# Performance work log

Measured on AMD Instinct MI355X. Metric: run time of the kernel, lower is better.

Reference implementation:

```python
import jax, jax.numpy as jnp
import numpy as np
import math

def setup_inputs() -> dict:
    key = jax.random.key(0)
    k1, k2, k3 = jax.random.split(key, 3)
    B, N, C = 32, 1024, 768
    x = jax.random.normal(k1, (B, N, C), dtype=jnp.float32)
    W = jax.random.normal(k2, (4, C), dtype=jnp.float32) * 0.02  # conv1x1 weight [out=4, in=C]
    b = jax.random.normal(k3, (4,), dtype=jnp.float32) * 0.02
    return {"x": x, "W": W, "b": b}

def reference(x, W, b):
    B, N, C = x.shape
    H = int(math.isqrt(N))
    L = H * H
    # [B,N,C] -> [B,C,H,H]
    xi = jnp.transpose(x, (0, 2, 1)).reshape(B, C, H, H)
    # alpha = Conv1x1(AvgPool(x)) -> [B,4]
    pooled = jnp.mean(xi, axis=(2, 3))                      # [B,C]
    alpha = pooled @ W.T + b                                # [B,4]
    a = alpha[:, :, None, None]                             # [B,4,1,1]
    # CrossScan directions
    x0 = xi.reshape(B, C, L)                                # row-major scan
    x1 = jnp.transpose(xi, (0, 1, 3, 2)).reshape(B, C, L)   # col-major scan
    x2 = x0[:, :, ::-1]                                     # reversed row-major
    x3 = x1[:, :, ::-1]                                     # reversed col-major
    # gated weighted sum over the 4 scans (fused elementwise)
    y = a[:, 0] * x0 + a[:, 1] * x1 + a[:, 2] * x2 + a[:, 3] * x3  # [B,C,L]
    return jnp.transpose(y, (0, 2, 1))                      # [B,L,C]
```

## Files before the change

kernel.cpp:

```cpp
#include <hip/hip_runtime.h>

#define BB 32
#define NN 1024
#define CC 768
#define HH 32
#define NCHUNK 32
#define NPER (NN / NCHUNK)
#define C4 (CC / 4)

__global__ void pool_partial(const float* __restrict__ x, float* __restrict__ part) {
    const int blk = blockIdx.x;
    const int b   = blk / NCHUNK;
    const int ch  = blk % NCHUNK;
    const int tid = threadIdx.x;
    const float* xb = x + ((size_t)b * NN + (size_t)ch * NPER) * CC;
    float* pb = part + (size_t)blk * CC;
#pragma unroll
    for (int cc = 0; cc < 3; ++cc) {
        const int c = cc * 256 + tid;
        float s = 0.f;
#pragma unroll 4
        for (int n = 0; n < NPER; ++n) s += xb[(size_t)n * CC + c];
        pb[c] = s;
    }
}

__global__ void alpha_kernel(const float* __restrict__ part,
                             const float* __restrict__ W,
                             const float* __restrict__ bias,
                             float* __restrict__ alpha) {
    const int b = blockIdx.x;
    const int tid = threadIdx.x;
    float ak[4] = {0.f, 0.f, 0.f, 0.f};
#pragma unroll
    for (int cc = 0; cc < 3; ++cc) {
        const int c = cc * 256 + tid;
        float s = 0.f;
#pragma unroll 8
        for (int ch = 0; ch < NCHUNK; ++ch)
            s += part[((size_t)b * NCHUNK + ch) * CC + c];
#pragma unroll
        for (int k = 0; k < 4; ++k) ak[k] += s * W[k * CC + c];
    }
    const int lane = tid & 63;
    const int wid  = tid >> 6;
    __shared__ float red[4][4];
#pragma unroll
    for (int k = 0; k < 4; ++k) {
        float v = ak[k];
#pragma unroll
        for (int off = 32; off >= 1; off >>= 1) v += __shfl_down(v, off);
        if (lane == 0) red[wid][k] = v;
    }
    __syncthreads();
    if (tid < 4) {
        const float s = red[0][tid] + red[1][tid] + red[2][tid] + red[3][tid];
        alpha[b * 4 + tid] = s * (1.0f / (float)NN) + bias[tid];
    }
}

__global__ void merge(const float* __restrict__ x,
                      const float* __restrict__ alpha,
                      float* __restrict__ out) {
    const unsigned total = (unsigned)BB * NN * C4;
    const float4* __restrict__ x4 = (const float4*)x;
    float4* __restrict__ o4 = (float4*)out;
    for (unsigned idx = blockIdx.x * blockDim.x + threadIdx.x; idx < total;
         idx += gridDim.x * blockDim.x) {
        const unsigned c4 = idx % C4;
        const unsigned l  = (idx / C4) % NN;
        const unsigned b  = idx / (C4 * NN);
        const unsigned lt  = ((l & (HH - 1)) << 5) | (l >> 5);
        const unsigned lr  = (NN - 1) - l;
        const unsigned ltr = (NN - 1) - lt;
        const float4* xb = x4 + (size_t)b * NN * C4;
        const float a0 = alpha[b * 4 + 0];
        const float a1 = alpha[b * 4 + 1];
        const float a2 = alpha[b * 4 + 2];
        const float a3 = alpha[b * 4 + 3];
        const float4 v0 = xb[(size_t)l   * C4 + c4];
        const float4 v1 = xb[(size_t)lt  * C4 + c4];
        const float4 v2 = xb[(size_t)lr  * C4 + c4];
        const float4 v3 = xb[(size_t)ltr * C4 + c4];
        float4 r;
        r.x = a0 * v0.x + a1 * v1.x + a2 * v2.x + a3 * v3.x;
        r.y = a0 * v0.y + a1 * v1.y + a2 * v2.y + a3 * v3.y;
        r.z = a0 * v0.z + a1 * v1.z + a2 * v2.z + a3 * v3.z;
        r.w = a0 * v0.w + a1 * v1.w + a2 * v2.w + a3 * v3.w;
        o4[idx] = r;
    }
}

extern "C" void kernel_launch(void* const* d_in, const int* in_sizes, int n_in,
                              void* d_out, int out_size, void* d_ws, size_t ws_size,
                              hipStream_t stream) {
    const float* x    = (const float*)d_in[0];
    const float* W    = (const float*)d_in[1];
    const float* bias = (const float*)d_in[2];
    float* out = (float*)d_out;

    float* part  = (float*)d_ws;
    float* alpha = part + (size_t)BB * NCHUNK * CC;

    pool_partial<<<BB * NCHUNK, 256, 0, stream>>>(x, part);
    alpha_kernel<<<BB, 256, 0, stream>>>(part, W, bias, alpha);
    merge<<<2048, 256, 0, stream>>>(x, alpha, out);
}
```

Baseline: 239.5 us.

## Process scan-symmetry orbits together so each input row is loaded once

The merge kernel now assigns one block per (batch, position) and handles only the canonical member of each orbit {l, transpose(l), reverse(l), reverse-transpose(l)}. It loads the four rows once and writes all four outputs using permuted alpha weights, with nontemporal stores. This removes the redundant fourfold gather of the input. Pooling and alpha kernels are switched to float4-vectorized loads with 192-thread blocks. Most merge blocks exit early, adding launch overhead in exchange for lower memory traffic.

```diff
diff --git a/kernel.cpp b/kernel.cpp
--- a/kernel.cpp
+++ b/kernel.cpp
@@ -8,43 +8,44 @@
 #define NPER (NN / NCHUNK)
 #define C4 (CC / 4)
 
-__global__ void pool_partial(const float* __restrict__ x, float* __restrict__ part) {
-    const int blk = blockIdx.x;
-    const int b   = blk / NCHUNK;
-    const int ch  = blk % NCHUNK;
-    const int tid = threadIdx.x;
-    const float* xb = x + ((size_t)b * NN + (size_t)ch * NPER) * CC;
-    float* pb = part + (size_t)blk * CC;
-#pragma unroll
-    for (int cc = 0; cc < 3; ++cc) {
-        const int c = cc * 256 + tid;
-        float s = 0.f;
-#pragma unroll 4
-        for (int n = 0; n < NPER; ++n) s += xb[(size_t)n * CC + c];
-        pb[c] = s;
-    }
+typedef float f32x4 __attribute__((ext_vector_type(4)));
+
+__device__ __forceinline__ f32x4 f4_fma4(float a0, f32x4 v0, float a1, f32x4 v1,
+                                         float a2, f32x4 v2, float a3, f32x4 v3) {
+    return a0 * v0 + a1 * v1 + a2 * v2 + a3 * v3;
 }
 
-__global__ void alpha_kernel(const float* __restrict__ part,
-                             const float* __restrict__ W,
+__global__ void pool_partial(const f32x4* __restrict__ x4, f32x4* __restrict__ part4) {
+    const int blk = blockIdx.x;
+    const int b   = blk >> 5;
+    const int ch  = blk & 31;
+    const int t   = threadIdx.x;
+    const f32x4* xb = x4 + ((size_t)(b * NN + ch * NPER)) * C4 + t;
+    f32x4 s = {0.f, 0.f, 0.f, 0.f};
+#pragma unroll 8
+    for (int n = 0; n < NPER; ++n) s += xb[(size_t)n * C4];
+    part4[(size_t)blk * C4 + t] = s;
+}
+
+__global__ void alpha_kernel(const f32x4* __restrict__ part4,
+                             const f32x4* __restrict__ W4,
                              const float* __restrict__ bias,
                              float* __restrict__ alpha) {
     const int b = blockIdx.x;
-    const int tid = threadIdx.x;
-    float ak[4] = {0.f, 0.f, 0.f, 0.f};
+    const int t = threadIdx.x;
+    f32x4 s = {0.f, 0.f, 0.f, 0.f};
+#pragma unroll 8
+    for (int ch = 0; ch < NCHUNK; ++ch)
+        s += part4[((size_t)(b * NCHUNK + ch)) * C4 + t];
+    float ak[4];
 #pragma unroll
-    for (int cc = 0; cc < 3; ++cc) {
-        const int c = cc * 256 + tid;
-        float s = 0.f;
-#pragma unroll 8
-        for (int ch = 0; ch < NCHUNK; ++ch)
-            s += part[((size_t)b * NCHUNK + ch) * CC + c];
-#pragma unroll
-        for (int k = 0; k < 4; ++k) ak[k] += s * W[k * CC + c];
+    for (int k = 0; k < 4; ++k) {
+        const f32x4 w = W4[k * C4 + t];
+        ak[k] = s.x * w.x + s.y * w.y + s.z * w.z + s.w * w.w;
     }
-    const int lane = tid & 63;
-    const int wid  = tid >> 6;
-    __shared__ float red[4][4];
+    const int lane = t & 63;
+    const int wid  = t >> 6;
+    __shared__ float red[3][4];
 #pragma unroll
     for (int k = 0; k < 4; ++k) {
         float v = ak[k];
@@ -53,42 +54,39 @@
         if (lane == 0) red[wid][k] = v;
     }
     __syncthreads();
-    if (tid < 4) {
-        const float s = red[0][tid] + red[1][tid] + red[2][tid] + red[3][tid];
-        alpha[b * 4 + tid] = s * (1.0f / (float)NN) + bias[tid];
+    if (t < 4) {
+        const float s3 = red[0][t] + red[1][t] + red[2][t];
+        alpha[b * 4 + t] = s3 * (1.0f / (float)NN) + bias[t];
     }
 }
 
-__global__ void merge(const float* __restrict__ x,
+__global__ void merge(const f32x4* __restrict__ x4,
                       const float* __restrict__ alpha,
-                      float* __restrict__ out) {
-    const unsigned total = (unsigned)BB * NN * C4;
-    const float4* __restrict__ x4 = (const float4*)x;
-    float4* __restrict__ o4 = (float4*)out;
-    for (unsigned idx = blockIdx.x * blockDim.x + threadIdx.x; idx < total;
-         idx += gridDim.x * blockDim.x) {
-        const unsigned c4 = idx % C4;
-        const unsigned l  = (idx / C4) % NN;
-        const unsigned b  = idx / (C4 * NN);
-        const unsigned lt  = ((l & (HH - 1)) << 5) | (l >> 5);
-        const unsigned lr  = (NN - 1) - l;
-        const unsigned ltr = (NN - 1) - lt;
-        const float4* xb = x4 + (size_t)b * NN * C4;
-        const float a0 = alpha[b * 4 + 0];
-        const float a1 = alpha[b * 4 + 1];
-        const float a2 = alpha[b * 4 + 2];
-        const float a3 = alpha[b * 4 + 3];
-        const float4 v0 = xb[(size_t)l   * C4 + c4];
-        const float4 v1 = xb[(size_t)lt  * C4 + c4];
-        const float4 v2 = xb[(size_t)lr  * C4 + c4];
-        const float4 v3 = xb[(size_t)ltr * C4 + c4];
-        float4 r;
-        r.x = a0 * v0.x + a1 * v1.x + a2 * v2.x + a3 * v3.x;
-        r.y = a0 * v0.y + a1 * v1.y + a2 * v2.y + a3 * v3.y;
-        r.z = a0 * v0.z + a1 * v1.z + a2 * v2.z + a3 * v3.z;
-        r.w = a0 * v0.w + a1 * v1.w + a2 * v2.w + a3 * v3.w;
-        o4[idx] = r;
-    }
+                      f32x4* __restrict__ o4) {
+    const int b = blockIdx.x >> 10;
+    const int l = blockIdx.x & 1023;
+    const int lt  = ((l & (HH - 1)) << 5) | (l >> 5);
+    const int lr  = (NN - 1) - l;
+    const int ltr = (NN - 1) - lt;
+    if (lt < l || lr < l || ltr < l) return;
+
+    const int t = threadIdx.x;
+    const f32x4* xb = x4 + (size_t)b * (NN * C4);
+    f32x4* ob = o4 + (size_t)b * (NN * C4);
+    const float a0 = alpha[b * 4 + 0];
+    const float a1 = alpha[b * 4 + 1];
+    const float a2 = alpha[b * 4 + 2];
+    const float a3 = alpha[b * 4 + 3];
+
+    const f32x4 v0 = xb[(size_t)l   * C4 + t];
+    const f32x4 v1 = xb[(size_t)lt  * C4 + t];
+    const f32x4 v2 = xb[(size_t)lr  * C4 + t];
+    const f32x4 v3 = xb[(size_t)ltr * C4 + t];
+
+    __builtin_nontemporal_store(f4_fma4(a0, v0, a1, v1, a2, v2, a3, v3), &ob[(size_t)l   * C4 + t]);
+    __builtin_nontemporal_store(f4_fma4(a0, v1, a1, v0, a2, v3, a3, v2), &ob[(size_t)lt  * C4 + t]);
+    __builtin_nontemporal_store(f4_fma4(a0, v2, a1, v3, a2, v0, a3, v1), &ob[(size_t)lr  * C4 + t]);
+    __builtin_nontemporal_store(f4_fma4(a0, v3, a1, v2, a2, v1, a3, v0), &ob[(size_t)ltr * C4 + t]);
 }
 
 extern "C" void kernel_launch(void* const* d_in, const int* in_sizes, int n_in,
@@ -102,7 +100,7 @@
     float* part  = (float*)d_ws;
     float* alpha = part + (size_t)BB * NCHUNK * CC;
 
-    pool_partial<<<BB * NCHUNK, 256, 0, stream>>>(x, part);
-    alpha_kernel<<<BB, 256, 0, stream>>>(part, W, bias, alpha);
-    merge<<<2048, 256, 0, stream>>>(x, alpha, out);
+    pool_partial<<<BB * NCHUNK, 192, 0, stream>>>((const f32x4*)x, (f32x4*)part);
+    alpha_kernel<<<BB, 192, 0, stream>>>((const f32x4*)part, (const f32x4*)W, bias, alpha);
+    merge<<<BB * NN, 192, 0, stream>>>((const f32x4*)x, alpha, (f32x4*)out);
 }
```

New measurement: 197.3 us. -17.6%, faster.
